# Kernel tuning notes

Hardware: AMD Instinct MI355X
Metric: run time of the kernel (lower is better)

Reference implementation:

```python
import jax, jax.numpy as jnp
import numpy as np

EPS = 1e-5


def conv2d(x, w, b, stride=1, pad=1):
    out = jax.lax.conv_general_dilated(
        x, w, (stride, stride), [(pad, pad), (pad, pad)],
        dimension_numbers=('NCHW', 'OIHW', 'NCHW'))
    return out + b[None, :, None, None]


def bn_inf(x, gamma, beta, mean, var):
    inv = gamma / jnp.sqrt(var + EPS)
    return x * inv[None, :, None, None] + (beta - mean * inv)[None, :, None, None]


def deform_conv(x, offset, weight, stride, pad, dil):
    # x: [B,Ci,H,W], offset: [B,2*K*K,Ho,Wo] (dy,dx interleaved per kernel pos),
    # weight: [Co,Ci,K,K]. torchvision DeformConv2d v1 semantics, no bias.
    B, Ci, H, W = x.shape
    Co, _, K, _ = weight.shape
    KK = K * K
    Ho = (H + 2 * pad - dil * (K - 1) - 1) // stride + 1
    Wo = (W + 2 * pad - dil * (K - 1) - 1) // stride + 1
    dy = offset[:, 0::2]  # [B,KK,Ho,Wo]
    dx = offset[:, 1::2]
    ky, kx = jnp.meshgrid(jnp.arange(K), jnp.arange(K), indexing='ij')
    ky = ky.reshape(KK).astype(x.dtype)
    kx = kx.reshape(KK).astype(x.dtype)
    base_y = (jnp.arange(Ho) * stride - pad).astype(x.dtype)
    base_x = (jnp.arange(Wo) * stride - pad).astype(x.dtype)
    ys = base_y[None, None, :, None] + (ky * dil)[None, :, None, None] + dy
    xs = base_x[None, None, None, :] + (kx * dil)[None, :, None, None] + dx
    y0 = jnp.floor(ys)
    x0 = jnp.floor(xs)
    fy = ys - y0
    fx = xs - x0

    def gather(img, iy, ix):
        # img: [Ci,H,W]; iy, ix: [KK,Ho,Wo] float integer-valued coords
        valid = (iy >= 0) & (iy < H) & (ix >= 0) & (ix < W)
        iyc = jnp.clip(iy, 0, H - 1).astype(jnp.int32)
        ixc = jnp.clip(ix, 0, W - 1).astype(jnp.int32)
        v = img[:, iyc, ixc]  # [Ci,KK,Ho,Wo]
        return v * valid[None].astype(img.dtype)

    def sample_one(img, y0b, x0b, fyb, fxb):
        w00 = (1 - fyb) * (1 - fxb)
        w01 = (1 - fyb) * fxb
        w10 = fyb * (1 - fxb)
        w11 = fyb * fxb
        s = (gather(img, y0b, x0b) * w00[None]
             + gather(img, y0b, x0b + 1) * w01[None]
             + gather(img, y0b + 1, x0b) * w10[None]
             + gather(img, y0b + 1, x0b + 1) * w11[None])
        return s  # [Ci,KK,Ho,Wo]

    sampled = jax.vmap(sample_one)(x, y0, x0, fy, fx)  # [B,Ci,KK,Ho,Wo]
    return jnp.einsum('oik,bikhw->bohw', weight.reshape(Co, Ci, KK), sampled)


def setup_inputs() -> dict:
    key = jax.random.key(0)
    ks = jax.random.split(key, 16)
    B, C, H, W = 8, 128, 64, 64
    d = dict(
        x=jax.random.normal(ks[0], (B, C, H, W), jnp.float32),
        w_off1=jax.random.normal(ks[1], (18, C, 3, 3), jnp.float32) * 0.01,
        b_off1=jnp.zeros((18,), jnp.float32),
        w_dc1=jax.random.normal(ks[2], (C, C, 3, 3), jnp.float32) * 0.05,
        g1=jnp.ones((C,), jnp.float32),
        beta1=jnp.zeros((C,), jnp.float32),
        m1=jax.random.normal(ks[3], (C,), jnp.float32) * 0.1,
        v1=jax.random.uniform(ks[4], (C,), jnp.float32) + 0.5,
        w_off2=jax.random.normal(ks[5], (18, C, 3, 3), jnp.float32) * 0.01,
        b_off2=jnp.zeros((18,), jnp.float32),
        w_dc2=jax.random.normal(ks[6], (C, C, 3, 3), jnp.float32) * 0.05,
        g2=jnp.ones((C,), jnp.float32),
        beta2=jnp.zeros((C,), jnp.float32),
        m2=jax.random.normal(ks[7], (C,), jnp.float32) * 0.1,
        v2=jax.random.uniform(ks[8], (C,), jnp.float32) + 0.5,
    )
    return d


def reference(x, w_off1, b_off1, w_dc1, g1, beta1, m1, v1,
              w_off2, b_off2, w_dc2, g2, beta2, m2, v2):
    # BasicBlock6 forward (stride=1, in_planes==planes => identity shortcut)
    off1 = conv2d(x, w_off1, b_off1, stride=1, pad=1)
    out = jax.nn.relu(bn_inf(deform_conv(x, off1, w_dc1, 1, 2, 2), g1, beta1, m1, v1))
    off2 = conv2d(out, w_off2, b_off2, stride=1, pad=1)
    out = bn_inf(deform_conv(out, off2, w_dc2, 1, 2, 2), g2, beta2, m2, v2)
    out = out + x  # identity shortcut
    return jax.nn.relu(out)
```

## Files before the change

### kernel.cpp

```cpp
#include <hip/hip_runtime.h>
#include <hip/hip_bf16.h>

#define CH   128
#define HH   64
#define WW   64
#define OFFC 18

typedef __attribute__((ext_vector_type(8))) short bf16x8;
typedef __attribute__((ext_vector_type(4))) short bf16x4;
typedef __attribute__((ext_vector_type(4))) float f32x4;

static __device__ __forceinline__ unsigned short f2bf(float f) {
    __hip_bfloat16 h = __float2bfloat16(f);
    return *reinterpret_cast<unsigned short*>(&h);
}
static __device__ __forceinline__ float bf2f(unsigned short u) {
    union { unsigned int i; float f; } x; x.i = ((unsigned int)u) << 16;
    return x.f;
}

__global__ __launch_bounds__(256) void prep_kernel(
    const float* __restrict__ x, unsigned short* __restrict__ xh,
    const float* __restrict__ wdc1, const float* __restrict__ wdc2,
    const float* __restrict__ wof1, const float* __restrict__ wof2,
    unsigned short* __restrict__ wpk1, unsigned short* __restrict__ wpk2,
    unsigned short* __restrict__ wpo1, unsigned short* __restrict__ wpo2)
{
    __shared__ float s[CH][WW + 1];
    int blk = blockIdx.x;
    int tid = threadIdx.x;

    if (blk < 1152) {
        const float* w = (blk < 576) ? wdc1 : wdc2;
        unsigned short* wp = (blk < 576) ? wpk1 : wpk2;
        int id = (blk % 576) * 256 + tid;
        int j    = id & 7;
        int lane = (id >> 3) & 63;
        int ot   = (id >> 9) & 7;
        int kk   = (id >> 12) & 3;
        int k    = id >> 14;
        int o = ot * 16 + (lane & 15);
        int i = kk * 32 + (lane >> 4) * 8 + j;
        wp[id] = f2bf(w[(o * CH + i) * 9 + k]);
        return;
    }
    if (blk < 1440) {
        const float* w = (blk < 1296) ? wof1 : wof2;
        unsigned short* wp = (blk < 1296) ? wpo1 : wpo2;
        int id = ((blk - 1152) % 144) * 256 + tid;
        int j    = id & 7;
        int lane = (id >> 3) & 63;
        int mt   = (id >> 9) & 1;
        int kk   = (id >> 10) & 3;
        int k    = id >> 12;
        int o = mt * 16 + (lane & 15);
        int i = kk * 32 + (lane >> 4) * 8 + j;
        wp[id] = (o < OFFC) ? f2bf(w[(o * CH + i) * 9 + k]) : (unsigned short)0;
        return;
    }

    int nb = blk - 1440;
    const float* xb = x + ((size_t)(nb >> 6) * CH * HH + (nb & 63)) * WW;

    int c_off = tid >> 4, w0 = (tid & 15) * 4;
    #pragma unroll
    for (int it = 0; it < 8; ++it) {
        int c = it * 16 + c_off;
        float4 vv = *(const float4*)&xb[(size_t)c * HH * WW + w0];
        s[c][w0] = vv.x; s[c][w0 + 1] = vv.y; s[c][w0 + 2] = vv.z; s[c][w0 + 3] = vv.w;
    }
    __syncthreads();

    int w = tid & 63, c0 = (tid >> 6) * 32;
    unsigned short* dst = xh + ((size_t)nb * WW + w) * CH + c0;
    unsigned short tmp[32];
    #pragma unroll
    for (int j = 0; j < 32; ++j) tmp[j] = f2bf(s[c0 + j][w]);
    #pragma unroll
    for (int q = 0; q < 4; ++q)
        *(bf16x8*)(dst + q * 8) = *(const bf16x8*)(tmp + q * 8);
}

__global__ __launch_bounds__(256) void off_conv_mfma_kernel(
    const unsigned short* __restrict__ xh,
    const unsigned short* __restrict__ wpo,
    const float* __restrict__ bias,
    unsigned short* __restrict__ offh)
{
    int wgid = blockIdx.x;
    int blk  = (wgid & 7) * 64 + (wgid >> 3);
    int b = blk >> 6, oh = blk & 63;
    int tid = threadIdx.x;
    int lane = tid & 63;
    int nt = tid >> 6;
    int nl = lane & 15;
    int kg = lane >> 4;

    f32x4 acc0 = {0.f, 0.f, 0.f, 0.f}, acc1 = {0.f, 0.f, 0.f, 0.f};
    const unsigned short* xb = xh + (size_t)b * HH * WW * CH;

    for (int k = 0; k < 9; ++k) {
        int ky = k / 3, kx = k - ky * 3;
        int ih = oh - 1 + ky;
        if (ih < 0 || ih >= HH) continue;
        int iw = nt * 16 + nl + kx - 1;
        bool valid = (iw >= 0) && (iw < WW);
        const unsigned short* row = xb + ((size_t)ih * WW + (valid ? iw : 0)) * CH + kg * 8;
        const unsigned short* wk = wpo + (size_t)k * 4096;
        #pragma unroll
        for (int kk = 0; kk < 4; ++kk) {
            bf16x8 bfrag = {0, 0, 0, 0, 0, 0, 0, 0};
            if (valid) bfrag = *(const bf16x8*)(row + kk * 32);
            bf16x8 a0 = *(const bf16x8*)(wk + (kk * 2 + 0) * 512 + lane * 8);
            bf16x8 a1 = *(const bf16x8*)(wk + (kk * 2 + 1) * 512 + lane * 8);
            acc0 = __builtin_amdgcn_mfma_f32_16x16x32_bf16(a0, bfrag, acc0, 0, 0, 0);
            acc1 = __builtin_amdgcn_mfma_f32_16x16x32_bf16(a1, bfrag, acc1, 0, 0, 0);
        }
    }

    int ow = nt * 16 + nl;
    #pragma unroll
    for (int r = 0; r < 4; ++r) {
        int co = kg * 4 + r;
        offh[(((size_t)b * OFFC + co) * HH + oh) * WW + ow] = f2bf(acc0[r] + bias[co]);
    }
    if (kg == 0) {
        #pragma unroll
        for (int r = 0; r < 2; ++r) {
            int co = 16 + r;
            offh[(((size_t)b * OFFC + co) * HH + oh) * WW + ow] = f2bf(acc1[r] + bias[co]);
        }
    }
}

__global__ __launch_bounds__(512, 4) void deform_row_kernel(
    const unsigned short* __restrict__ xh,
    const unsigned short* __restrict__ offh,
    const unsigned short* __restrict__ wpk,
    const float* __restrict__ g, const float* __restrict__ beta,
    const float* __restrict__ m, const float* __restrict__ v,
    const float* __restrict__ residual,
    unsigned short* __restrict__ out_h,
    float* __restrict__ out_f)
{
    __shared__ unsigned short sB[64 * 128];
    __shared__ float off_s[OFFC][WW];

    int wgid = blockIdx.x;
    int blk  = (wgid & 7) * 64 + (wgid >> 3);
    int b = blk >> 6, oh = blk & 63;
    int tid = threadIdx.x, lane = tid & 63, wv = tid >> 6;

    int s_ow = tid >> 3;
    int ci0  = (tid & 7) * 16;

    const unsigned short* xb = xh + (size_t)b * HH * WW * CH;

    for (int i = tid; i < OFFC * WW; i += 512) {
        int co = i >> 6, owl = i & 63;
        off_s[co][owl] =
            bf2f(offh[(((size_t)b * OFFC + co) * HH + oh) * WW + owl]);
    }
    __syncthreads();

    f32x4 acc[4];
    #pragma unroll
    for (int q = 0; q < 4; ++q) acc[q] = (f32x4){0.f, 0.f, 0.f, 0.f};

    for (int k = 0; k < 9; ++k) {
        int ky = k / 3, kx = k - ky * 3;

        float dy = off_s[2 * k][s_ow];
        float dx = off_s[2 * k + 1][s_ow];
        float ys = (float)(oh - 2 + ky * 2) + dy;
        float xs = (float)(s_ow - 2 + kx * 2) + dx;
        float y0f = floorf(ys), x0f = floorf(xs);
        float fy = ys - y0f, fx = xs - x0f;
        int y0 = (int)y0f, x0i = (int)x0f;
        int y1 = y0 + 1, x1 = x0i + 1;
        bool vy0 = (y0 >= 0) & (y0 < HH), vy1 = (y1 >= 0) & (y1 < HH);
        bool vx0 = (x0i >= 0) & (x0i < WW), vx1 = (x1 >= 0) & (x1 < WW);
        int y0c = min(max(y0, 0), HH - 1), y1c = min(max(y1, 0), HH - 1);
        int x0c = min(max(x0i, 0), WW - 1), x1c = min(max(x1, 0), WW - 1);
        float cw0 = (1.f - fy) * (1.f - fx) * ((vy0 && vx0) ? 1.f : 0.f);
        float cw1 = (1.f - fy) * fx         * ((vy0 && vx1) ? 1.f : 0.f);
        float cw2 = fy * (1.f - fx)         * ((vy1 && vx0) ? 1.f : 0.f);
        float cw3 = fy * fx                 * ((vy1 && vx1) ? 1.f : 0.f);

        const unsigned short* p0 = xb + ((size_t)(y0c * WW + x0c)) * CH + ci0;
        const unsigned short* p1 = xb + ((size_t)(y0c * WW + x1c)) * CH + ci0;
        const unsigned short* p2 = xb + ((size_t)(y1c * WW + x0c)) * CH + ci0;
        const unsigned short* p3 = xb + ((size_t)(y1c * WW + x1c)) * CH + ci0;

        int base = s_ow * 256 + ci0 * 2;
        int swz  = (s_ow & 7) << 4;
        #pragma unroll
        for (int q = 0; q < 2; ++q) {
            bf16x8 g0 = *(const bf16x8*)(p0 + q * 8);
            bf16x8 g1 = *(const bf16x8*)(p1 + q * 8);
            bf16x8 g2 = *(const bf16x8*)(p2 + q * 8);
            bf16x8 g3 = *(const bf16x8*)(p3 + q * 8);
            union { bf16x8 v8; unsigned short u[8]; } wu;
            #pragma unroll
            for (int j = 0; j < 8; ++j) {
                float val = cw0 * bf2f((unsigned short)g0[j])
                          + cw1 * bf2f((unsigned short)g1[j])
                          + cw2 * bf2f((unsigned short)g2[j])
                          + cw3 * bf2f((unsigned short)g3[j]);
                wu.u[j] = f2bf(val);
            }
            *(bf16x8*)((char*)sB + ((base + q * 16) ^ swz)) = wu.v8;
        }
        __syncthreads();

        const unsigned short* wk = wpk + (size_t)k * 16384;
        #pragma unroll
        for (int kk = 0; kk < 4; ++kk) {
            bf16x8 a = *(const bf16x8*)(wk + (size_t)(kk * 8 + wv) * 512 + lane * 8);
            #pragma unroll
            for (int owt = 0; owt < 4; ++owt) {
                int owl = owt * 16 + (lane & 15);
                int rbyte = (owl * 256 + (kk * 32 + (lane >> 4) * 8) * 2)
                            ^ ((owl & 7) << 4);
                bf16x8 bfv = *(const bf16x8*)((const char*)sB + rbyte);
                acc[owt] = __builtin_amdgcn_mfma_f32_16x16x32_bf16(
                               a, bfv, acc[owt], 0, 0, 0);
            }
        }
        __syncthreads();
    }

    int ob = wv * 16 + (lane >> 4) * 4;
    float inv[4], sh[4];
    #pragma unroll
    for (int r = 0; r < 4; ++r) {
        int o = ob + r;
        float iv = g[o] / sqrtf(v[o] + 1e-5f);
        inv[r] = iv; sh[r] = beta[o] - m[o] * iv;
    }

    if (out_h != nullptr) {
        #pragma unroll
        for (int owt = 0; owt < 4; ++owt) {
            int ow = owt * 16 + (lane & 15);
            union { bf16x4 v4; unsigned short u[4]; } pk;
            #pragma unroll
            for (int r = 0; r < 4; ++r) {
                float val = acc[owt][r] * inv[r] + sh[r];
                pk.u[r] = f2bf(fmaxf(val, 0.f));
            }
            *(bf16x4*)(out_h + ((size_t)(b * HH + oh) * WW + ow) * CH + ob) = pk.v4;
        }
    } else {
        #pragma unroll
        for (int r = 0; r < 4; ++r) {
            int o = ob + r;
            #pragma unroll
            for (int owt = 0; owt < 4; ++owt) {
                int ow = owt * 16 + (lane & 15);
                size_t idx = (((size_t)b * CH + o) * HH + oh) * WW + ow;
                float val = acc[owt][r] * inv[r] + sh[r] + residual[idx];
                out_f[idx] = fmaxf(val, 0.f);
            }
        }
    }
}

extern "C" void kernel_launch(void* const* d_in, const int* in_sizes, int n_in,
                              void* d_out, int out_size, void* d_ws, size_t ws_size,
                              hipStream_t stream)
{
    const float* x      = (const float*)d_in[0];
    const float* w_off1 = (const float*)d_in[1];
    const float* b_off1 = (const float*)d_in[2];
    const float* w_dc1  = (const float*)d_in[3];
    const float* g1     = (const float*)d_in[4];
    const float* beta1  = (const float*)d_in[5];
    const float* m1     = (const float*)d_in[6];
    const float* v1     = (const float*)d_in[7];
    const float* w_off2 = (const float*)d_in[8];
    const float* b_off2 = (const float*)d_in[9];
    const float* w_dc2  = (const float*)d_in[10];
    const float* g2     = (const float*)d_in[11];
    const float* beta2  = (const float*)d_in[12];
    const float* m2     = (const float*)d_in[13];
    const float* v2     = (const float*)d_in[14];
    float* out = (float*)d_out;

    char* ws = (char*)d_ws;
    unsigned short* xh    = (unsigned short*)ws;
    unsigned short* out1h = (unsigned short*)(ws + 8388608);
    unsigned short* offh  = (unsigned short*)(ws + 16777216);
    unsigned short* wpk1  = (unsigned short*)(ws + 17956864);
    unsigned short* wpk2  = (unsigned short*)(ws + 18251776);
    unsigned short* wpo1  = (unsigned short*)(ws + 18546688);
    unsigned short* wpo2  = (unsigned short*)(ws + 18620416);

    prep_kernel<<<1952, 256, 0, stream>>>(x, xh, w_dc1, w_dc2, w_off1, w_off2,
                                          wpk1, wpk2, wpo1, wpo2);

    off_conv_mfma_kernel<<<512, 256, 0, stream>>>(xh, wpo1, b_off1, offh);
    deform_row_kernel<<<512, 512, 0, stream>>>(xh, offh, wpk1,
                                               g1, beta1, m1, v1,
                                               nullptr, out1h, nullptr);
    off_conv_mfma_kernel<<<512, 256, 0, stream>>>(out1h, wpo2, b_off2, offh);
    deform_row_kernel<<<512, 512, 0, stream>>>(out1h, offh, wpk2,
                                               g2, beta2, m2, v2,
                                               x, nullptr, out);
}
```

Baseline: 95.20 us.

## Warp-specialize deform conv into producer gather and consumer MFMA waves

```diff
diff --git a/kernel.cpp b/kernel.cpp
--- a/kernel.cpp
+++ b/kernel.cpp
@@ -133,7 +133,7 @@
     }
 }
 
-__global__ __launch_bounds__(512, 4) void deform_row_kernel(
+__global__ __launch_bounds__(512, 4) void deform_pc_kernel(
     const unsigned short* __restrict__ xh,
     const unsigned short* __restrict__ offh,
     const unsigned short* __restrict__ wpk,
@@ -143,17 +143,15 @@
     unsigned short* __restrict__ out_h,
     float* __restrict__ out_f)
 {
-    __shared__ unsigned short sB[64 * 128];
+    __shared__ unsigned short sB[2][64 * 128];
     __shared__ float off_s[OFFC][WW];
+    __shared__ int flg[4];
 
     int wgid = blockIdx.x;
     int blk  = (wgid & 7) * 64 + (wgid >> 3);
     int b = blk >> 6, oh = blk & 63;
     int tid = threadIdx.x, lane = tid & 63, wv = tid >> 6;
 
-    int s_ow = tid >> 3;
-    int ci0  = (tid & 7) * 16;
-
     const unsigned short* xb = xh + (size_t)b * HH * WW * CH;
 
     for (int i = tid; i < OFFC * WW; i += 512) {
@@ -161,106 +159,148 @@
         off_s[co][owl] =
             bf2f(offh[(((size_t)b * OFFC + co) * HH + oh) * WW + owl]);
     }
+    if (tid < 4) flg[tid] = 0;
     __syncthreads();
 
-    f32x4 acc[4];
-    #pragma unroll
-    for (int q = 0; q < 4; ++q) acc[q] = (f32x4){0.f, 0.f, 0.f, 0.f};
-
-    for (int k = 0; k < 9; ++k) {
-        int ky = k / 3, kx = k - ky * 3;
-
-        float dy = off_s[2 * k][s_ow];
-        float dx = off_s[2 * k + 1][s_ow];
-        float ys = (float)(oh - 2 + ky * 2) + dy;
-        float xs = (float)(s_ow - 2 + kx * 2) + dx;
-        float y0f = floorf(ys), x0f = floorf(xs);
-        float fy = ys - y0f, fx = xs - x0f;
-        int y0 = (int)y0f, x0i = (int)x0f;
-        int y1 = y0 + 1, x1 = x0i + 1;
-        bool vy0 = (y0 >= 0) & (y0 < HH), vy1 = (y1 >= 0) & (y1 < HH);
-        bool vx0 = (x0i >= 0) & (x0i < WW), vx1 = (x1 >= 0) & (x1 < WW);
-        int y0c = min(max(y0, 0), HH - 1), y1c = min(max(y1, 0), HH - 1);
-        int x0c = min(max(x0i, 0), WW - 1), x1c = min(max(x1, 0), WW - 1);
-        float cw0 = (1.f - fy) * (1.f - fx) * ((vy0 && vx0) ? 1.f : 0.f);
-        float cw1 = (1.f - fy) * fx         * ((vy0 && vx1) ? 1.f : 0.f);
-        float cw2 = fy * (1.f - fx)         * ((vy1 && vx0) ? 1.f : 0.f);
-        float cw3 = fy * fx                 * ((vy1 && vx1) ? 1.f : 0.f);
-
-        const unsigned short* p0 = xb + ((size_t)(y0c * WW + x0c)) * CH + ci0;
-        const unsigned short* p1 = xb + ((size_t)(y0c * WW + x1c)) * CH + ci0;
-        const unsigned short* p2 = xb + ((size_t)(y1c * WW + x0c)) * CH + ci0;
-        const unsigned short* p3 = xb + ((size_t)(y1c * WW + x1c)) * CH + ci0;
-
-        int base = s_ow * 256 + ci0 * 2;
-        int swz  = (s_ow & 7) << 4;
+    if (wv < 4) {
+        int s_ow = tid >> 3;
+        int cig  = tid & 7;
+
+        for (int k = 0; k < 9; ++k) {
+            int buf = k & 1;
+            if (k >= 2) {
+                int tgt = 4 * (k >> 1);
+                while (__hip_atomic_load(&flg[2 + buf], __ATOMIC_ACQUIRE,
+                                         __HIP_MEMORY_SCOPE_WORKGROUP) < tgt)
+                    __builtin_amdgcn_s_sleep(1);
+            }
+            int ky = k / 3, kx = k - ky * 3;
+
+            #pragma unroll
+            for (int w2 = 0; w2 < 2; ++w2) {
+                int ow = s_ow + w2 * 32;
+                float dy = off_s[2 * k][ow];
+                float dx = off_s[2 * k + 1][ow];
+                float ys = (float)(oh - 2 + ky * 2) + dy;
+                float xs = (float)(ow - 2 + kx * 2) + dx;
+                float y0f = floorf(ys), x0f = floorf(xs);
+                float fy = ys - y0f, fx = xs - x0f;
+                int y0 = (int)y0f, x0i = (int)x0f;
+                int y1 = y0 + 1, x1 = x0i + 1;
+                bool vy0 = (y0 >= 0) & (y0 < HH), vy1 = (y1 >= 0) & (y1 < HH);
+                bool vx0 = (x0i >= 0) & (x0i < WW), vx1 = (x1 >= 0) & (x1 < WW);
+                int y0c = min(max(y0, 0), HH - 1), y1c = min(max(y1, 0), HH - 1);
+                int x0c = min(max(x0i, 0), WW - 1), x1c = min(max(x1, 0), WW - 1);
+                float cw0 = (1.f - fy) * (1.f - fx) * ((vy0 && vx0) ? 1.f : 0.f);
+                float cw1 = (1.f - fy) * fx         * ((vy0 && vx1) ? 1.f : 0.f);
+                float cw2 = fy * (1.f - fx)         * ((vy1 && vx0) ? 1.f : 0.f);
+                float cw3 = fy * fx                 * ((vy1 && vx1) ? 1.f : 0.f);
+
+                const unsigned short* p0 = xb + ((size_t)(y0c * WW + x0c)) * CH + cig * 8;
+                const unsigned short* p1 = xb + ((size_t)(y0c * WW + x1c)) * CH + cig * 8;
+                const unsigned short* p2 = xb + ((size_t)(y1c * WW + x0c)) * CH + cig * 8;
+                const unsigned short* p3 = xb + ((size_t)(y1c * WW + x1c)) * CH + cig * 8;
+
+                int swz = (ow & 7) << 4;
+                #pragma unroll
+                for (int q = 0; q < 2; ++q) {
+                    int cie = q * 64 + cig * 8;
+                    bf16x8 g0 = *(const bf16x8*)(p0 + q * 64);
+                    bf16x8 g1 = *(const bf16x8*)(p1 + q * 64);
+                    bf16x8 g2 = *(const bf16x8*)(p2 + q * 64);
+                    bf16x8 g3 = *(const bf16x8*)(p3 + q * 64);
+                    union { bf16x8 v8; unsigned short u[8]; } wu;
+                    #pragma unroll
+                    for (int j = 0; j < 8; ++j) {
+                        float val = cw0 * bf2f((unsigned short)g0[j])
+                                  + cw1 * bf2f((unsigned short)g1[j])
+                                  + cw2 * bf2f((unsigned short)g2[j])
+                                  + cw3 * bf2f((unsigned short)g3[j]);
+                        wu.u[j] = f2bf(val);
+                    }
+                    int byte = (ow * 256 + cie * 2) ^ swz;
+                    *(bf16x8*)((char*)sB[buf] + byte) = wu.v8;
+                }
+            }
+            asm volatile("s_waitcnt lgkmcnt(0)" ::: "memory");
+            if (lane == 0)
+                __hip_atomic_fetch_add(&flg[buf], 1, __ATOMIC_RELEASE,
+                                       __HIP_MEMORY_SCOPE_WORKGROUP);
+        }
+    } else {
+        int cw = wv - 4;
+        f32x4 acc[2][4];
         #pragma unroll
-        for (int q = 0; q < 2; ++q) {
-            bf16x8 g0 = *(const bf16x8*)(p0 + q * 8);
-            bf16x8 g1 = *(const bf16x8*)(p1 + q * 8);
-            bf16x8 g2 = *(const bf16x8*)(p2 + q * 8);
-            bf16x8 g3 = *(const bf16x8*)(p3 + q * 8);
-            union { bf16x8 v8; unsigned short u[8]; } wu;
+        for (int a = 0; a < 2; ++a)
             #pragma unroll
-            for (int j = 0; j < 8; ++j) {
-                float val = cw0 * bf2f((unsigned short)g0[j])
-                          + cw1 * bf2f((unsigned short)g1[j])
-                          + cw2 * bf2f((unsigned short)g2[j])
-                          + cw3 * bf2f((unsigned short)g3[j]);
-                wu.u[j] = f2bf(val);
-            }
-            *(bf16x8*)((char*)sB + ((base + q * 16) ^ swz)) = wu.v8;
-        }
-        __syncthreads();
-
-        const unsigned short* wk = wpk + (size_t)k * 16384;
+            for (int q = 0; q < 4; ++q) acc[a][q] = (f32x4){0.f, 0.f, 0.f, 0.f};
+
+        for (int k = 0; k < 9; ++k) {
+            int buf = k & 1;
+            int tgt = 4 * ((k >> 1) + 1);
+            while (__hip_atomic_load(&flg[buf], __ATOMIC_ACQUIRE,
+                                     __HIP_MEMORY_SCOPE_WORKGROUP) < tgt)
+                __builtin_amdgcn_s_sleep(1);
+
+            const unsigned short* wk = wpk + (size_t)k * 16384;
+            __builtin_amdgcn_s_setprio(1);
+            #pragma unroll
+            for (int kk = 0; kk < 4; ++kk) {
+                bf16x8 a0 = *(const bf16x8*)(wk + (size_t)(kk * 8 + 2 * cw)     * 512 + lane * 8);
+                bf16x8 a1 = *(const bf16x8*)(wk + (size_t)(kk * 8 + 2 * cw + 1) * 512 + lane * 8);
+                #pragma unroll
+                for (int owt = 0; owt < 4; ++owt) {
+                    int owl = owt * 16 + (lane & 15);
+                    int rbyte = (owl * 256 + (kk * 32 + (lane >> 4) * 8) * 2)
+                                ^ ((owl & 7) << 4);
+                    bf16x8 bfv = *(const bf16x8*)((const char*)sB[buf] + rbyte);
+                    acc[0][owt] = __builtin_amdgcn_mfma_f32_16x16x32_bf16(
+                                      a0, bfv, acc[0][owt], 0, 0, 0);
+                    acc[1][owt] = __builtin_amdgcn_mfma_f32_16x16x32_bf16(
+                                      a1, bfv, acc[1][owt], 0, 0, 0);
+                }
+            }
+            __builtin_amdgcn_s_setprio(0);
+            asm volatile("s_waitcnt lgkmcnt(0)" ::: "memory");
+            if (lane == 0)
+                __hip_atomic_fetch_add(&flg[2 + buf], 1, __ATOMIC_RELEASE,
+                                       __HIP_MEMORY_SCOPE_WORKGROUP);
+        }
+
         #pragma unroll
-        for (int kk = 0; kk < 4; ++kk) {
-            bf16x8 a = *(const bf16x8*)(wk + (size_t)(kk * 8 + wv) * 512 + lane * 8);
-            #pragma unroll
-            for (int owt = 0; owt < 4; ++owt) {
-                int owl = owt * 16 + (lane & 15);
-                int rbyte = (owl * 256 + (kk * 32 + (lane >> 4) * 8) * 2)
-                            ^ ((owl & 7) << 4);
-                bf16x8 bfv = *(const bf16x8*)((const char*)sB + rbyte);
-                acc[owt] = __builtin_amdgcn_mfma_f32_16x16x32_bf16(
-                               a, bfv, acc[owt], 0, 0, 0);
-            }
-        }
-        __syncthreads();
-    }
-
-    int ob = wv * 16 + (lane >> 4) * 4;
-    float inv[4], sh[4];
-    #pragma unroll
-    for (int r = 0; r < 4; ++r) {
-        int o = ob + r;
-        float iv = g[o] / sqrtf(v[o] + 1e-5f);
-        inv[r] = iv; sh[r] = beta[o] - m[o] * iv;
-    }
-
-    if (out_h != nullptr) {
-        #pragma unroll
-        for (int owt = 0; owt < 4; ++owt) {
-            int ow = owt * 16 + (lane & 15);
-            union { bf16x4 v4; unsigned short u[4]; } pk;
+        for (int otl = 0; otl < 2; ++otl) {
+            int ob = (2 * cw + otl) * 16 + (lane >> 4) * 4;
+            float inv[4], sh[4];
             #pragma unroll
             for (int r = 0; r < 4; ++r) {
-                float val = acc[owt][r] * inv[r] + sh[r];
-                pk.u[r] = f2bf(fmaxf(val, 0.f));
-            }
-            *(bf16x4*)(out_h + ((size_t)(b * HH + oh) * WW + ow) * CH + ob) = pk.v4;
-        }
-    } else {
-        #pragma unroll
-        for (int r = 0; r < 4; ++r) {
-            int o = ob + r;
-            #pragma unroll
-            for (int owt = 0; owt < 4; ++owt) {
-                int ow = owt * 16 + (lane & 15);
-                size_t idx = (((size_t)b * CH + o) * HH + oh) * WW + ow;
-                float val = acc[owt][r] * inv[r] + sh[r] + residual[idx];
-                out_f[idx] = fmaxf(val, 0.f);
+                int o = ob + r;
+                float iv = g[o] / sqrtf(v[o] + 1e-5f);
+                inv[r] = iv; sh[r] = beta[o] - m[o] * iv;
+            }
+            if (out_h != nullptr) {
+                #pragma unroll
+                for (int owt = 0; owt < 4; ++owt) {
+                    int ow = owt * 16 + (lane & 15);
+                    union { bf16x4 v4; unsigned short u[4]; } pk;
+                    #pragma unroll
+                    for (int r = 0; r < 4; ++r) {
+                        float val = acc[otl][owt][r] * inv[r] + sh[r];
+                        pk.u[r] = f2bf(fmaxf(val, 0.f));
+                    }
+                    *(bf16x4*)(out_h + ((size_t)(b * HH + oh) * WW + ow) * CH + ob) = pk.v4;
+                }
+            } else {
+                #pragma unroll
+                for (int r = 0; r < 4; ++r) {
+                    int o = ob + r;
+                    #pragma unroll
+                    for (int owt = 0; owt < 4; ++owt) {
+                        int ow = owt * 16 + (lane & 15);
+                        size_t idx = (((size_t)b * CH + o) * HH + oh) * WW + ow;
+                        float val = acc[otl][owt][r] * inv[r] + sh[r] + residual[idx];
+                        out_f[idx] = fmaxf(val, 0.f);
+                    }
+                }
             }
         }
     }
@@ -300,11 +340,11 @@
                                           wpk1, wpk2, wpo1, wpo2);
 
     off_conv_mfma_kernel<<<512, 256, 0, stream>>>(xh, wpo1, b_off1, offh);
-    deform_row_kernel<<<512, 512, 0, stream>>>(xh, offh, wpk1,
-                                               g1, beta1, m1, v1,
-                                               nullptr, out1h, nullptr);
+    deform_pc_kernel<<<512, 512, 0, stream>>>(xh, offh, wpk1,
+                                              g1, beta1, m1, v1,
+                                              nullptr, out1h, nullptr);
     off_conv_mfma_kernel<<<512, 256, 0, stream>>>(out1h, wpo2, b_off2, offh);
-    deform_row_kernel<<<512, 512, 0, stream>>>(out1h, offh, wpk2,
-                                               g2, beta2, m2, v2,
-                                               x, nullptr, out);
-}
+    deform_pc_kernel<<<512, 512, 0, stream>>>(out1h, offh, wpk2,
+                                              g2, beta2, m2, v2,
+                                              x, nullptr, out);
+}
```

Result: faster. 91.56 us (-3.8%).
